# Kernel tuning notes

Hardware: AMD Instinct MI355X
Metric: run time of the kernel (lower is better)

Reference implementation:

```python
import jax, jax.numpy as jnp
import numpy as np

NEG_INF = -1e9  # stands in for the eye(W)*sys.maxsize self-mask on the row axis


def setup_inputs() -> dict:
    key = jax.random.key(0)
    ks = jax.random.split(key, 8)
    B, C, S = 8, 512, 128
    C8 = C // 8
    sc = 0.02
    x = jax.random.normal(ks[0], (B, C, S, S), dtype=jnp.float32)
    Wq = jax.random.normal(ks[1], (C8, C), dtype=jnp.float32) * sc
    bq = jnp.zeros((C8,), dtype=jnp.float32)
    Wk = jax.random.normal(ks[2], (C8, C), dtype=jnp.float32) * sc
    bk = jnp.zeros((C8,), dtype=jnp.float32)
    Wv = jax.random.normal(ks[3], (C, C), dtype=jnp.float32) * sc
    bv = jnp.zeros((C,), dtype=jnp.float32)
    gamma = jnp.ones((1,), dtype=jnp.float32) * 0.5  # source inits to 0; nonzero so path is exercised
    return {"x": x, "Wq": Wq, "bq": bq, "Wk": Wk, "bk": bk, "Wv": Wv, "bv": bv, "gamma": gamma}


def reference(x, Wq, bq, Wk, bk, Wv, bv, gamma):
    # x: (B, C, W, H) with W == H == S (required by the eye-mask view in the source)
    B, C, S, _ = x.shape
    # 1x1 convs = per-pixel linear projections
    q = jnp.einsum('oc,bcwh->bowh', Wq, x) + bq[None, :, None, None]  # (B,C8,S,S)
    k = jnp.einsum('oc,bcwh->bowh', Wk, x) + bk[None, :, None, None]
    v = jnp.einsum('oc,bcwh->bowh', Wv, x) + bv[None, :, None, None]  # (B,C,S,S)

    # column ('h'-fixed) attention along W, self position masked out
    e_col = jnp.einsum('bcwh,bcuh->bwhu', q, k)  # (B,W,H,W)
    self_mask = jnp.eye(S, dtype=bool)  # w == u
    e_col = jnp.where(self_mask[None, :, None, :], NEG_INF, e_col)
    # row ('w'-fixed) attention along H
    e_row = jnp.einsum('bcwh,bcwu->bwhu', q, k)  # (B,W,H,H)

    att = jax.nn.softmax(jnp.concatenate([e_col, e_row], axis=-1), axis=-1)  # (B,W,H,2S)
    a_col = att[..., :S]   # weights over w'
    a_row = att[..., S:]   # weights over h'

    out = (jnp.einsum('bwhu,bcuh->bcwh', a_col, v)
           + jnp.einsum('bwhu,bcwu->bcwh', a_row, v))  # (B,C,S,S)
    return gamma[0] * out + x
```

## Files before the change

kernel.cpp:

```cpp
#include <hip/hip_runtime.h>
#include <hip/hip_bf16.h>


#define S 128
#define SS 16384
#define C 512
#define C8 64
#define NEG_BIG -1000000000.0f

using short8 = __attribute__((ext_vector_type(8))) short;
using f32x4  = __attribute__((ext_vector_type(4))) float;

#define GPTR(p) ((const __attribute__((address_space(1))) void*)(p))
#define LPTR(p) ((__attribute__((address_space(3))) void*)(p))

__device__ __forceinline__ unsigned short f2b(float f){
  union { float f; unsigned u; } v; v.f = f;
  unsigned r = (v.u + 0x7fffu + ((v.u >> 16) & 1u)) >> 16;
  return (unsigned short)r;
}
__device__ __forceinline__ float b2f(unsigned short h){
  union { unsigned u; float f; } v; v.u = ((unsigned)h) << 16;
  return v.f;
}

__device__ __forceinline__ void stage_tile64(unsigned short* dst,
    const unsigned short* src, int tid){
  #pragma unroll
  for (int p = 0; p < 4; ++p){
    int gi = p * 256 + tid;
    int row = gi >> 3, cc = gi & 7;
    int kc = (cc ^ (row & 7)) * 8;
    __builtin_amdgcn_global_load_lds(GPTR(src + (size_t)row * C + kc),
                                     LPTR((char*)dst + gi * 16), 16, 0, 0);
  }
}

__global__ __launch_bounds__(256) void k_pack_w(
    const float* __restrict__ Wq, const float* __restrict__ Wk,
    const float* __restrict__ Wv, unsigned short* __restrict__ wall){
  int i = blockIdx.x * 256 + threadIdx.x;
  if (i >= 640 * C) return;
  int co = i >> 9, ci = i & (C - 1);
  float v;
  if (co < 64)        v = Wq[co * C + ci];
  else if (co < 128)  v = Wk[(co - 64) * C + ci];
  else                v = Wv[(co - 128) * C + ci];
  wall[i] = f2b(v);
}

__global__ __launch_bounds__(256) void k_xp(
    const float* __restrict__ x, unsigned short* __restrict__ xp){
  __shared__ unsigned short T[128 * 130] __attribute__((aligned(16)));
  int blk = blockIdx.x;
  int ct = blk & 3; int bw = blk >> 2;
  int w = bw & 127; int b = bw >> 7;
  int tid = threadIdx.x;
  int ci0 = ct * 128;
  const float* xb = x + ((size_t)(b * C + ci0) * S + w) * S;
  #pragma unroll
  for (int p = 0; p < 16; ++p){
    int idx = p * 256 + tid;
    int cc = idx >> 5;
    int h4 = (idx & 31) * 4;
    float4 v = *(const float4*)(xb + (size_t)cc * SS + h4);
    unsigned* d = (unsigned*)&T[cc * 130 + h4];
    d[0] = (unsigned)f2b(v.x) | ((unsigned)f2b(v.y) << 16);
    d[1] = (unsigned)f2b(v.z) | ((unsigned)f2b(v.w) << 16);
  }
  __syncthreads();
  unsigned short* xpb = xp + (size_t)(b * S + w) * S * C + ci0;
  #pragma unroll
  for (int p = 0; p < 8; ++p){
    int idx = p * 256 + tid;
    int h  = idx >> 4;
    int ch = (idx & 15) * 8;
    unsigned short tmp[8] __attribute__((aligned(16)));
    #pragma unroll
    for (int j = 0; j < 8; ++j) tmp[j] = T[(ch + j) * 130 + h];
    *(uint4*)(xpb + (size_t)h * C + ch) = *(uint4*)tmp;
  }
}

__global__ __launch_bounds__(256) void k_qkv(
    const unsigned short* __restrict__ xp, const unsigned short* __restrict__ wall,
    const float* __restrict__ bq, const float* __restrict__ bk,
    const float* __restrict__ bv,
    unsigned short* __restrict__ qp, unsigned short* __restrict__ kp,
    unsigned short* __restrict__ vb){
  __shared__ unsigned short sm[32768] __attribute__((aligned(16)));
  unsigned short* Dl = sm;
  int blk = blockIdx.x;
  int pxsub = blk & 7; int t = blk >> 3;
  int cot = t % 5; int pxg = t / 5;
  int pxt = pxg * 8 + pxsub;
  int w = pxt & 127, b = pxt >> 7;
  int tid = threadIdx.x, lane = tid & 63, wid = tid >> 6;
  int qd = lane >> 4, ln = lane & 15;
  const unsigned short* asrc0 = wall + (size_t)cot * 128 * C;
  const unsigned short* bsrc0 = xp + (size_t)pxt * 128 * C;
  f32x4 acc[4][4];
  #pragma unroll
  for (int i = 0; i < 4; ++i)
    #pragma unroll
    for (int j = 0; j < 4; ++j) acc[i][j] = (f32x4){0.f, 0.f, 0.f, 0.f};

  stage_tile64(sm,        asrc0, tid);
  stage_tile64(sm + 8192, bsrc0, tid);
  __syncthreads();

  for (int kw = 0; kw < 8; ++kw){
    unsigned short* Acur = sm + (kw & 1) * 16384;
    unsigned short* Bcur = Acur + 8192;
    if (kw < 7){
      unsigned short* Anxt = sm + ((kw + 1) & 1) * 16384;
      stage_tile64(Anxt,        asrc0 + (kw + 1) * 64, tid);
      stage_tile64(Anxt + 8192, bsrc0 + (kw + 1) * 64, tid);
    }
    __builtin_amdgcn_s_setprio(1);
    #pragma unroll
    for (int ks = 0; ks < 2; ++ks){
      int ch8 = (((ks * 4 + qd) ^ (ln & 7)) * 8);
      short8 af[4], bfr[4];
      #pragma unroll
      for (int i = 0; i < 4; ++i)
        af[i] = *(const short8*)&Acur[(((wid & 1) * 4 + i) * 16 + ln) * 64 + ch8];
      #pragma unroll
      for (int j = 0; j < 4; ++j)
        bfr[j] = *(const short8*)&Bcur[(((wid >> 1) * 4 + j) * 16 + ln) * 64 + ch8];
      #pragma unroll
      for (int i = 0; i < 4; ++i)
        #pragma unroll
        for (int j = 0; j < 4; ++j)
          acc[i][j] = __builtin_amdgcn_mfma_f32_16x16x32_bf16(af[i], bfr[j], acc[i][j], 0, 0, 0);
    }
    __builtin_amdgcn_s_setprio(0);
    __syncthreads();
  }
  float bias_[4][4];
  #pragma unroll
  for (int i = 0; i < 4; ++i){
    int co_l0 = ((wid & 1) * 4 + i) * 16 + qd * 4;
    #pragma unroll
    for (int r = 0; r < 4; ++r){
      int co_l = co_l0 + r;
      bias_[i][r] = (cot == 0) ? (co_l < 64 ? bq[co_l] : bk[co_l - 64])
                               : bv[(cot - 1) * 128 + co_l];
    }
  }
  #pragma unroll
  for (int i = 0; i < 4; ++i){
    int co_l0 = ((wid & 1) * 4 + i) * 16 + qd * 4;
    #pragma unroll
    for (int j = 0; j < 4; ++j){
      int pxl = ((wid >> 1) * 4 + j) * 16 + ln;
      #pragma unroll
      for (int r = 0; r < 4; ++r)
        Dl[(co_l0 + r) * 136 + pxl] = f2b(acc[i][j][r] + bias_[i][r]);
    }
  }
  __syncthreads();
  if (cot == 0){
    unsigned short* qb = qp + (size_t)(b * S + w) * S * C8;
    unsigned short* kb = kp + (size_t)(b * S + w) * S * C8;
    #pragma unroll
    for (int p = 0; p < 4; ++p){
      int idx = p * 256 + tid;
      int cch = idx & 7, hh = idx >> 3;
      unsigned short tq[8] __attribute__((aligned(16)));
      unsigned short tk[8] __attribute__((aligned(16)));
      #pragma unroll
      for (int jj = 0; jj < 8; ++jj){
        tq[jj] = Dl[(cch * 8 + jj) * 136 + hh];
        tk[jj] = Dl[(64 + cch * 8 + jj) * 136 + hh];
      }
      *(uint4*)(qb + (size_t)hh * C8 + cch * 8) = *(uint4*)tq;
      *(uint4*)(kb + (size_t)hh * C8 + cch * 8) = *(uint4*)tk;
    }
  } else {
    unsigned short* vbb = vb + ((size_t)(b * C + (cot - 1) * 128) * S + w) * S;
    #pragma unroll
    for (int p = 0; p < 8; ++p){
      int idx = p * 256 + tid;
      int c_l = idx >> 4, hc = (idx & 15) * 8;
      uint4 v = *(const uint4*)&Dl[c_l * 136 + hc];
      *(uint4*)(vbb + (size_t)c_l * SS + hc) = v;
    }
  }
}

__global__ __launch_bounds__(256) void k_tv(
    const unsigned short* __restrict__ vb, unsigned short* __restrict__ vt){
  __shared__ unsigned short T[128 * 130] __attribute__((aligned(16)));
  int bc = blockIdx.x;
  const unsigned short* src = vb + (size_t)bc * SS;
  unsigned short* dst = vt + (size_t)bc * SS;
  int tid = threadIdx.x;
  #pragma unroll
  for (int p = 0; p < 8; ++p){
    int idx = p * 256 + tid;
    int wv = idx >> 4, ch = (idx & 15) * 8;
    uint4 v = *(const uint4*)(src + wv * S + ch);
    unsigned* d = (unsigned*)&T[wv * 130 + ch];
    d[0] = v.x; d[1] = v.y; d[2] = v.z; d[3] = v.w;
  }
  __syncthreads();
  #pragma unroll
  for (int p = 0; p < 8; ++p){
    int idx = p * 256 + tid;
    int h = idx >> 4, ch = (idx & 15) * 8;
    unsigned short tmp[8] __attribute__((aligned(16)));
    #pragma unroll
    for (int j = 0; j < 8; ++j) tmp[j] = T[(ch + j) * 130 + h];
    *(uint4*)(dst + h * S + ch) = *(uint4*)tmp;
  }
}

__global__ __launch_bounds__(256) void k_ecol(
    const unsigned short* __restrict__ qp, const unsigned short* __restrict__ kp,
    unsigned short* __restrict__ eca){
  __shared__ unsigned short Aq[128 * 72] __attribute__((aligned(16)));
  __shared__ unsigned short Bk[128 * 72] __attribute__((aligned(16)));
  int blk = blockIdx.x; int h = blk & 127, b = blk >> 7;
  int tid = threadIdx.x, lane = tid & 63, wid = tid >> 6;
  int qd = lane >> 4, ln = lane & 15;
  #pragma unroll
  for (int p = 0; p < 4; ++p){
    int idx = p * 256 + tid;
    int row = idx >> 3, ch = (idx & 7) * 8;
    *(uint4*)&Aq[row * 72 + ch] = *(const uint4*)(qp + ((size_t)(b * S + row) * S + h) * C8 + ch);
    *(uint4*)&Bk[row * 72 + ch] = *(const uint4*)(kp + ((size_t)(b * S + row) * S + h) * C8 + ch);
  }
  __syncthreads();
  f32x4 acc[4][4];
  #pragma unroll
  for (int i = 0; i < 4; ++i)
    #pragma unroll
    for (int j = 0; j < 4; ++j) acc[i][j] = (f32x4){0.f, 0.f, 0.f, 0.f};
  #pragma unroll
  for (int ks = 0; ks < 2; ++ks){
    int ko = ks * 32 + qd * 8;
    short8 af[4], bfr[4];
    #pragma unroll
    for (int i = 0; i < 4; ++i)
      af[i] = *(const short8*)&Aq[(((wid & 1) * 4 + i) * 16 + ln) * 72 + ko];
    #pragma unroll
    for (int j = 0; j < 4; ++j)
      bfr[j] = *(const short8*)&Bk[(((wid >> 1) * 4 + j) * 16 + ln) * 72 + ko];
    #pragma unroll
    for (int i = 0; i < 4; ++i)
      #pragma unroll
      for (int j = 0; j < 4; ++j)
        acc[i][j] = __builtin_amdgcn_mfma_f32_16x16x32_bf16(af[i], bfr[j], acc[i][j], 0, 0, 0);
  }
  #pragma unroll
  for (int i = 0; i < 4; ++i){
    int w0 = ((wid & 1) * 4 + i) * 16 + qd * 4;
    #pragma unroll
    for (int j = 0; j < 4; ++j){
      int ug = ((wid >> 1) * 4 + j) * 16 + ln;
      #pragma unroll
      for (int r = 0; r < 4; ++r){
        int wg = w0 + r;
        float val = acc[i][j][r];
        if (wg == ug) val = NEG_BIG;
        eca[((size_t)(b * S + wg) * S + h) * S + ug] = f2b(val);
      }
    }
  }
}

__global__ __launch_bounds__(256) void k_erow_softmax(
    const unsigned short* __restrict__ qp, const unsigned short* __restrict__ kp,
    unsigned short* __restrict__ eca, unsigned short* __restrict__ ar){
  __shared__ char sm[36864] __attribute__((aligned(16)));
  unsigned short* Aq = (unsigned short*)sm;
  unsigned short* Bk = (unsigned short*)(sm + 18432);
  unsigned short* El = (unsigned short*)sm;
  float* redm = (float*)(sm + 34816);
  float* reds = (float*)(sm + 35840);
  int blk = blockIdx.x; int w = blk & 127, b = blk >> 7;
  int tid = threadIdx.x, lane = tid & 63, wid = tid >> 6;
  int qd = lane >> 4, ln = lane & 15;
  size_t tb = (size_t)(b * S + w) * SS;
  {
    const unsigned short* qsrc = qp + (size_t)(b * S + w) * S * C8;
    const unsigned short* ksrc = kp + (size_t)(b * S + w) * S * C8;
    #pragma unroll
    for (int p = 0; p < 4; ++p){
      int idx = p * 256 + tid;
      int row = idx >> 3, ch = (idx & 7) * 8;
      *(uint4*)&Aq[row * 72 + ch] = *(const uint4*)(qsrc + row * C8 + ch);
      *(uint4*)&Bk[row * 72 + ch] = *(const uint4*)(ksrc + row * C8 + ch);
    }
  }
  __syncthreads();
  f32x4 acc[4][4];
  #pragma unroll
  for (int i = 0; i < 4; ++i)
    #pragma unroll
    for (int j = 0; j < 4; ++j) acc[i][j] = (f32x4){0.f, 0.f, 0.f, 0.f};
  #pragma unroll
  for (int ks = 0; ks < 2; ++ks){
    int ko = ks * 32 + qd * 8;
    short8 af[4], bfr[4];
    #pragma unroll
    for (int i = 0; i < 4; ++i)
      af[i] = *(const short8*)&Aq[(((wid & 1) * 4 + i) * 16 + ln) * 72 + ko];
    #pragma unroll
    for (int j = 0; j < 4; ++j)
      bfr[j] = *(const short8*)&Bk[(((wid >> 1) * 4 + j) * 16 + ln) * 72 + ko];
    #pragma unroll
    for (int i = 0; i < 4; ++i)
      #pragma unroll
      for (int j = 0; j < 4; ++j)
        acc[i][j] = __builtin_amdgcn_mfma_f32_16x16x32_bf16(af[i], bfr[j], acc[i][j], 0, 0, 0);
  }
  __syncthreads();
  #pragma unroll
  for (int i = 0; i < 4; ++i){
    int h0 = ((wid & 1) * 4 + i) * 16 + qd * 4;
    #pragma unroll
    for (int j = 0; j < 4; ++j){
      int ul = ((wid >> 1) * 4 + j) * 16 + ln;
      #pragma unroll
      for (int r = 0; r < 4; ++r)
        El[(h0 + r) * 136 + ul] = f2b(acc[i][j][r]);
    }
  }
  __syncthreads();
  int h = tid >> 1, half = tid & 1;
  const uint4* src4 = (half == 0) ? (const uint4*)(eca + tb + (size_t)h * S)
                                  : (const uint4*)&El[h * 136];
  float mx = -3.0e38f;
  #pragma unroll 4
  for (int u = 0; u < 16; ++u){
    uint4 v = src4[u];
    const unsigned short* e = (const unsigned short*)&v;
    #pragma unroll
    for (int jj = 0; jj < 8; ++jj) mx = fmaxf(mx, b2f(e[jj]));
  }
  redm[tid] = mx;
  __syncthreads();
  float m = fmaxf(mx, redm[tid ^ 1]);
  float s = 0.f;
  #pragma unroll 4
  for (int u = 0; u < 16; ++u){
    uint4 v = src4[u];
    const unsigned short* e = (const unsigned short*)&v;
    #pragma unroll
    for (int jj = 0; jj < 8; ++jj) s += __expf(b2f(e[jj]) - m);
  }
  reds[tid] = s;
  __syncthreads();
  float inv = 1.0f / (s + reds[tid ^ 1]);
  uint4* dst4 = (half == 0) ? (uint4*)(eca + tb + (size_t)h * S)
                            : (uint4*)(ar + tb + (size_t)h * S);
  #pragma unroll 4
  for (int u = 0; u < 16; ++u){
    uint4 v = src4[u];
    const unsigned short* e = (const unsigned short*)&v;
    unsigned short o[8] __attribute__((aligned(16)));
    #pragma unroll
    for (int jj = 0; jj < 8; ++jj) o[jj] = f2b(__expf(b2f(e[jj]) - m) * inv);
    dst4[u] = *(uint4*)o;
  }
}

__global__ __launch_bounds__(256) void k_outrow(
    const unsigned short* __restrict__ vb, const unsigned short* __restrict__ ar,
    unsigned short* __restrict__ orw){
  __shared__ unsigned short Av[128 * 72] __attribute__((aligned(16)));
  __shared__ unsigned short Ba[128 * 72] __attribute__((aligned(16)));
  int blk = blockIdx.x;
  int ct = blk & 3; int bw = blk >> 2;
  int w = bw & 127, b = bw >> 7;
  int tid = threadIdx.x, lane = tid & 63, wid = tid >> 6;
  int qd = lane >> 4, ln = lane & 15;
  size_t tb = (size_t)(b * S + w) * SS;
  f32x4 acc[4][4];
  #pragma unroll
  for (int i = 0; i < 4; ++i)
    #pragma unroll
    for (int j = 0; j < 4; ++j) acc[i][j] = (f32x4){0.f, 0.f, 0.f, 0.f};
  for (int kw = 0; kw < 2; ++kw){
    __syncthreads();
    #pragma unroll
    for (int p = 0; p < 4; ++p){
      int idx = p * 256 + tid;
      int row = idx >> 3, ch = (idx & 7) * 8;
      *(uint4*)&Av[row * 72 + ch] =
        *(const uint4*)(vb + ((size_t)(b * C + ct * 128 + row) * S + w) * S + kw * 64 + ch);
      *(uint4*)&Ba[row * 72 + ch] =
        *(const uint4*)(ar + tb + (size_t)row * S + kw * 64 + ch);
    }
    __syncthreads();
    #pragma unroll
    for (int ks = 0; ks < 2; ++ks){
      int ko = ks * 32 + qd * 8;
      short8 af[4], bfr[4];
      #pragma unroll
      for (int i = 0; i < 4; ++i)
        af[i] = *(const short8*)&Av[(((wid & 1) * 4 + i) * 16 + ln) * 72 + ko];
      #pragma unroll
      for (int j = 0; j < 4; ++j)
        bfr[j] = *(const short8*)&Ba[(((wid >> 1) * 4 + j) * 16 + ln) * 72 + ko];
      #pragma unroll
      for (int i = 0; i < 4; ++i)
        #pragma unroll
        for (int j = 0; j < 4; ++j)
          acc[i][j] = __builtin_amdgcn_mfma_f32_16x16x32_bf16(af[i], bfr[j], acc[i][j], 0, 0, 0);
    }
  }
  #pragma unroll
  for (int i = 0; i < 4; ++i){
    int c0 = ((wid & 1) * 4 + i) * 16 + qd * 4;
    #pragma unroll
    for (int j = 0; j < 4; ++j){
      int hl = ((wid >> 1) * 4 + j) * 16 + ln;
      #pragma unroll
      for (int r = 0; r < 4; ++r){
        int cg = ct * 128 + c0 + r;
        orw[((size_t)(b * C + cg) * S + w) * S + hl] = f2b(acc[i][j][r]);
      }
    }
  }
}

__global__ __launch_bounds__(256) void k_outcol(
    const unsigned short* __restrict__ vt, const unsigned short* __restrict__ eca,
    unsigned short* __restrict__ oct){
  __shared__ unsigned short Av[128 * 72] __attribute__((aligned(16)));
  __shared__ unsigned short Ba[128 * 72] __attribute__((aligned(16)));
  int blk = blockIdx.x;
  int ct = blk & 3; int bh = blk >> 2;
  int h = bh & 127, b = bh >> 7;
  int tid = threadIdx.x, lane = tid & 63, wid = tid >> 6;
  int qd = lane >> 4, ln = lane & 15;
  f32x4 acc[4][4];
  #pragma unroll
  for (int i = 0; i < 4; ++i)
    #pragma unroll
    for (int j = 0; j < 4; ++j) acc[i][j] = (f32x4){0.f, 0.f, 0.f, 0.f};
  for (int kw = 0; kw < 2; ++kw){
    __syncthreads();
    #pragma unroll
    for (int p = 0; p < 4; ++p){
      int idx = p * 256 + tid;
      int row = idx >> 3, ch = (idx & 7) * 8;
      *(uint4*)&Av[row * 72 + ch] =
        *(const uint4*)(vt + ((size_t)(b * C + ct * 128 + row) * S + h) * S + kw * 64 + ch);
      *(uint4*)&Ba[row * 72 + ch] =
        *(const uint4*)(eca + ((size_t)(b * S + row) * S + h) * S + kw * 64 + ch);
    }
    __syncthreads();
    #pragma unroll
    for (int ks = 0; ks < 2; ++ks){
      int ko = ks * 32 + qd * 8;
      short8 af[4], bfr[4];
      #pragma unroll
      for (int i = 0; i < 4; ++i)
        af[i] = *(const short8*)&Av[(((wid & 1) * 4 + i) * 16 + ln) * 72 + ko];
      #pragma unroll
      for (int j = 0; j < 4; ++j)
        bfr[j] = *(const short8*)&Ba[(((wid >> 1) * 4 + j) * 16 + ln) * 72 + ko];
      #pragma unroll
      for (int i = 0; i < 4; ++i)
        #pragma unroll
        for (int j = 0; j < 4; ++j)
          acc[i][j] = __builtin_amdgcn_mfma_f32_16x16x32_bf16(af[i], bfr[j], acc[i][j], 0, 0, 0);
    }
  }
  #pragma unroll
  for (int i = 0; i < 4; ++i){
    int c0 = ((wid & 1) * 4 + i) * 16 + qd * 4;
    #pragma unroll
    for (int j = 0; j < 4; ++j){
      int wl = ((wid >> 1) * 4 + j) * 16 + ln;
      #pragma unroll
      for (int r = 0; r < 4; ++r){
        int cg = ct * 128 + c0 + r;
        oct[((size_t)(b * S + h) * C + cg) * S + wl] = f2b(acc[i][j][r]);
      }
    }
  }
}

__global__ __launch_bounds__(256) void k_final(
    const unsigned short* __restrict__ oct, const unsigned short* __restrict__ orw,
    const float* __restrict__ x, const float* __restrict__ gamma,
    float* __restrict__ out){
  __shared__ unsigned short T[128 * 130] __attribute__((aligned(16)));
  int blk = blockIdx.x;
  int c = blk & 511, b = blk >> 9;
  int tid = threadIdx.x;
  float g = gamma[0];
  #pragma unroll
  for (int p = 0; p < 8; ++p){
    int idx = p * 256 + tid;
    int hh = idx >> 4, ch = (idx & 15) * 8;
    uint4 v = *(const uint4*)(oct + ((size_t)(b * S + hh) * C + c) * S + ch);
    unsigned* d = (unsigned*)&T[hh * 130 + ch];
    d[0] = v.x; d[1] = v.y; d[2] = v.z; d[3] = v.w;
  }
  __syncthreads();
  #pragma unroll
  for (int p = 0; p < 8; ++p){
    int idx = p * 256 + tid;
    int wv = idx >> 4, hch = (idx & 15) * 8;
    size_t o = ((size_t)(b * C + c) * S + wv) * S + hch;
    uint4 rv = *(const uint4*)(orw + o);
    const unsigned short* rr = (const unsigned short*)&rv;
    float4 x0 = *(const float4*)(x + o);
    float4 x1 = *(const float4*)(x + o + 4);
    float4 o0, o1;
    o0.x = g * (b2f(rr[0]) + b2f(T[(hch + 0) * 130 + wv])) + x0.x;
    o0.y = g * (b2f(rr[1]) + b2f(T[(hch + 1) * 130 + wv])) + x0.y;
    o0.z = g * (b2f(rr[2]) + b2f(T[(hch + 2) * 130 + wv])) + x0.z;
    o0.w = g * (b2f(rr[3]) + b2f(T[(hch + 3) * 130 + wv])) + x0.w;
    o1.x = g * (b2f(rr[4]) + b2f(T[(hch + 4) * 130 + wv])) + x1.x;
    o1.y = g * (b2f(rr[5]) + b2f(T[(hch + 5) * 130 + wv])) + x1.y;
    o1.z = g * (b2f(rr[6]) + b2f(T[(hch + 6) * 130 + wv])) + x1.z;
    o1.w = g * (b2f(rr[7]) + b2f(T[(hch + 7) * 130 + wv])) + x1.w;
    *(float4*)(out + o) = o0;
    *(float4*)(out + o + 4) = o1;
  }
}

extern "C" void kernel_launch(void* const* d_in, const int* in_sizes, int n_in,
                              void* d_out, int out_size, void* d_ws, size_t ws_size,
                              hipStream_t stream){
  const float* x     = (const float*)d_in[0];
  const float* Wq    = (const float*)d_in[1];
  const float* bq    = (const float*)d_in[2];
  const float* Wk    = (const float*)d_in[3];
  const float* bk    = (const float*)d_in[4];
  const float* Wv    = (const float*)d_in[5];
  const float* bv    = (const float*)d_in[6];
  const float* gamma = (const float*)d_in[7];
  float* out = (float*)d_out;
  char* ws = (char*)d_ws;

  const size_t OFF_WALL = 0;
  const size_t OFF_XP   = 1ull << 20;
  const size_t OFF_QP   = OFF_XP  + 134217728ull;
  const size_t OFF_KP   = OFF_QP  + 16777216ull;
  const size_t OFF_VB   = OFF_KP  + 16777216ull;
  const size_t OFF_VT   = OFF_VB  + 134217728ull;
  const size_t OFF_ECA  = OFF_VT  + 134217728ull;
  const size_t OFF_AR   = OFF_ECA + 33554432ull;
  const size_t OFF_OCT  = OFF_XP;
  const size_t OFF_ORW  = OFF_VT;
  const size_t NEED     = OFF_AR + 33554432ull;
  if (ws_size < NEED) return;

  unsigned short* wall = (unsigned short*)(ws + OFF_WALL);
  unsigned short* xp   = (unsigned short*)(ws + OFF_XP);
  unsigned short* qp   = (unsigned short*)(ws + OFF_QP);
  unsigned short* kp   = (unsigned short*)(ws + OFF_KP);
  unsigned short* vb   = (unsigned short*)(ws + OFF_VB);
  unsigned short* vt   = (unsigned short*)(ws + OFF_VT);
  unsigned short* eca  = (unsigned short*)(ws + OFF_ECA);
  unsigned short* ar   = (unsigned short*)(ws + OFF_AR);
  unsigned short* oct  = (unsigned short*)(ws + OFF_OCT);
  unsigned short* orw  = (unsigned short*)(ws + OFF_ORW);

  k_pack_w      <<<1280, 256, 0, stream>>>(Wq, Wk, Wv, wall);
  k_xp          <<<4096, 256, 0, stream>>>(x, xp);
  k_qkv         <<<5120, 256, 0, stream>>>(xp, wall, bq, bk, bv, qp, kp, vb);
  k_tv          <<<4096, 256, 0, stream>>>(vb, vt);
  k_ecol        <<<1024, 256, 0, stream>>>(qp, kp, eca);
  k_erow_softmax<<<1024, 256, 0, stream>>>(qp, kp, eca, ar);
  k_outcol      <<<4096, 256, 0, stream>>>(vt, eca, oct);
  k_outrow      <<<4096, 256, 0, stream>>>(vb, ar, orw);
  k_final       <<<4096, 256, 0, stream>>>(oct, orw, x, gamma, out);
}
```

Baseline: 987.6 us.

## Fuse row softmax with row-attention output GEMM and permute transpose rows

The row-energy softmax kernel now keeps the normalized row attention weights in shared memory and immediately runs the V·A_row GEMM across all channel tiles. V tiles are double-buffered via global_load_lds, and the result is written in place over vb. This removes the separate k_outrow launch, the round trip of the `ar` buffer through global memory, and the repeated reloads of attention weights. Separately, the LDS transpose buffers use a row permutation (PR) to reduce bank conflicts. The costs are roughly 70KB of LDS per block, which lowers occupancy, and in-place overwriting of vb that depends on each block reading only its own w-slice.

```diff
diff --git a/kernel.cpp b/kernel.cpp
--- a/kernel.cpp
+++ b/kernel.cpp
@@ -14,6 +14,8 @@
 #define GPTR(p) ((const __attribute__((address_space(1))) void*)(p))
 #define LPTR(p) ((__attribute__((address_space(3))) void*)(p))
 
+#define PR(r) ((((r) & 7) << 4) | ((r) >> 3))
+
 __device__ __forceinline__ unsigned short f2b(float f){
   union { float f; unsigned u; } v; v.f = f;
   unsigned r = (v.u + 0x7fffu + ((v.u >> 16) & 1u)) >> 16;
@@ -25,13 +27,13 @@
 }
 
 __device__ __forceinline__ void stage_tile64(unsigned short* dst,
-    const unsigned short* src, int tid){
+    const unsigned short* src, size_t rstride, int tid){
   #pragma unroll
   for (int p = 0; p < 4; ++p){
     int gi = p * 256 + tid;
     int row = gi >> 3, cc = gi & 7;
     int kc = (cc ^ (row & 7)) * 8;
-    __builtin_amdgcn_global_load_lds(GPTR(src + (size_t)row * C + kc),
+    __builtin_amdgcn_global_load_lds(GPTR(src + (size_t)row * rstride + kc),
                                      LPTR((char*)dst + gi * 16), 16, 0, 0);
   }
 }
@@ -64,7 +66,7 @@
     int cc = idx >> 5;
     int h4 = (idx & 31) * 4;
     float4 v = *(const float4*)(xb + (size_t)cc * SS + h4);
-    unsigned* d = (unsigned*)&T[cc * 130 + h4];
+    unsigned* d = (unsigned*)&T[PR(cc) * 130 + h4];
     d[0] = (unsigned)f2b(v.x) | ((unsigned)f2b(v.y) << 16);
     d[1] = (unsigned)f2b(v.z) | ((unsigned)f2b(v.w) << 16);
   }
@@ -77,7 +79,7 @@
     int ch = (idx & 15) * 8;
     unsigned short tmp[8] __attribute__((aligned(16)));
     #pragma unroll
-    for (int j = 0; j < 8; ++j) tmp[j] = T[(ch + j) * 130 + h];
+    for (int j = 0; j < 8; ++j) tmp[j] = T[PR(ch + j) * 130 + h];
     *(uint4*)(xpb + (size_t)h * C + ch) = *(uint4*)tmp;
   }
 }
@@ -105,8 +107,8 @@
     #pragma unroll
     for (int j = 0; j < 4; ++j) acc[i][j] = (f32x4){0.f, 0.f, 0.f, 0.f};
 
-  stage_tile64(sm,        asrc0, tid);
-  stage_tile64(sm + 8192, bsrc0, tid);
+  stage_tile64(sm,        asrc0, C, tid);
+  stage_tile64(sm + 8192, bsrc0, C, tid);
   __syncthreads();
 
   for (int kw = 0; kw < 8; ++kw){
@@ -114,8 +116,8 @@
     unsigned short* Bcur = Acur + 8192;
     if (kw < 7){
       unsigned short* Anxt = sm + ((kw + 1) & 1) * 16384;
-      stage_tile64(Anxt,        asrc0 + (kw + 1) * 64, tid);
-      stage_tile64(Anxt + 8192, bsrc0 + (kw + 1) * 64, tid);
+      stage_tile64(Anxt,        asrc0 + (kw + 1) * 64, C, tid);
+      stage_tile64(Anxt + 8192, bsrc0 + (kw + 1) * 64, C, tid);
     }
     __builtin_amdgcn_s_setprio(1);
     #pragma unroll
@@ -201,7 +203,7 @@
     int idx = p * 256 + tid;
     int wv = idx >> 4, ch = (idx & 15) * 8;
     uint4 v = *(const uint4*)(src + wv * S + ch);
-    unsigned* d = (unsigned*)&T[wv * 130 + ch];
+    unsigned* d = (unsigned*)&T[PR(wv) * 130 + ch];
     d[0] = v.x; d[1] = v.y; d[2] = v.z; d[3] = v.w;
   }
   __syncthreads();
@@ -211,7 +213,7 @@
     int h = idx >> 4, ch = (idx & 15) * 8;
     unsigned short tmp[8] __attribute__((aligned(16)));
     #pragma unroll
-    for (int j = 0; j < 8; ++j) tmp[j] = T[(ch + j) * 130 + h];
+    for (int j = 0; j < 8; ++j) tmp[j] = T[PR(ch + j) * 130 + h];
     *(uint4*)(dst + h * S + ch) = *(uint4*)tmp;
   }
 }
@@ -270,19 +272,23 @@
   }
 }
 
-__global__ __launch_bounds__(256) void k_erow_softmax(
+__global__ __launch_bounds__(256) void k_erow_sm_outrow(
     const unsigned short* __restrict__ qp, const unsigned short* __restrict__ kp,
-    unsigned short* __restrict__ eca, unsigned short* __restrict__ ar){
-  __shared__ char sm[36864] __attribute__((aligned(16)));
-  unsigned short* Aq = (unsigned short*)sm;
-  unsigned short* Bk = (unsigned short*)(sm + 18432);
-  unsigned short* El = (unsigned short*)sm;
-  float* redm = (float*)(sm + 34816);
-  float* reds = (float*)(sm + 35840);
+    unsigned short* __restrict__ eca, unsigned short* vb){
+  __shared__ char sm[71680] __attribute__((aligned(16)));
+  unsigned short* Aq  = (unsigned short*)sm;
+  unsigned short* Bk  = (unsigned short*)(sm + 18432);
+  unsigned short* El  = (unsigned short*)sm;
+  unsigned short* Av0 = (unsigned short*)(sm + 36864);
+  unsigned short* Av1 = (unsigned short*)(sm + 53248);
+  float* redm = (float*)(sm + 69632);
+  float* reds = (float*)(sm + 70656);
   int blk = blockIdx.x; int w = blk & 127, b = blk >> 7;
   int tid = threadIdx.x, lane = tid & 63, wid = tid >> 6;
   int qd = lane >> 4, ln = lane & 15;
   size_t tb = (size_t)(b * S + w) * SS;
+  const unsigned short* vsrc0 = vb + (size_t)(b * C) * SS + (size_t)w * S;
+
   {
     const unsigned short* qsrc = qp + (size_t)(b * S + w) * S * C8;
     const unsigned short* ksrc = kp + (size_t)(b * S + w) * S * C8;
@@ -294,6 +300,7 @@
       *(uint4*)&Bk[row * 72 + ch] = *(const uint4*)(ksrc + row * C8 + ch);
     }
   }
+  stage_tile64(Av0, vsrc0, SS, tid);
   __syncthreads();
   f32x4 acc[4][4];
   #pragma unroll
@@ -329,101 +336,95 @@
     }
   }
   __syncthreads();
-  int h = tid >> 1, half = tid & 1;
-  const uint4* src4 = (half == 0) ? (const uint4*)(eca + tb + (size_t)h * S)
-                                  : (const uint4*)&El[h * 136];
-  float mx = -3.0e38f;
-  #pragma unroll 4
-  for (int u = 0; u < 16; ++u){
-    uint4 v = src4[u];
-    const unsigned short* e = (const unsigned short*)&v;
-    #pragma unroll
-    for (int jj = 0; jj < 8; ++jj) mx = fmaxf(mx, b2f(e[jj]));
-  }
-  redm[tid] = mx;
-  __syncthreads();
-  float m = fmaxf(mx, redm[tid ^ 1]);
-  float s = 0.f;
-  #pragma unroll 4
-  for (int u = 0; u < 16; ++u){
-    uint4 v = src4[u];
-    const unsigned short* e = (const unsigned short*)&v;
-    #pragma unroll
-    for (int jj = 0; jj < 8; ++jj) s += __expf(b2f(e[jj]) - m);
-  }
-  reds[tid] = s;
-  __syncthreads();
-  float inv = 1.0f / (s + reds[tid ^ 1]);
-  uint4* dst4 = (half == 0) ? (uint4*)(eca + tb + (size_t)h * S)
-                            : (uint4*)(ar + tb + (size_t)h * S);
-  #pragma unroll 4
-  for (int u = 0; u < 16; ++u){
-    uint4 v = src4[u];
-    const unsigned short* e = (const unsigned short*)&v;
-    unsigned short o[8] __attribute__((aligned(16)));
-    #pragma unroll
-    for (int jj = 0; jj < 8; ++jj) o[jj] = f2b(__expf(b2f(e[jj]) - m) * inv);
-    dst4[u] = *(uint4*)o;
-  }
-}
-
-__global__ __launch_bounds__(256) void k_outrow(
-    const unsigned short* __restrict__ vb, const unsigned short* __restrict__ ar,
-    unsigned short* __restrict__ orw){
-  __shared__ unsigned short Av[128 * 72] __attribute__((aligned(16)));
-  __shared__ unsigned short Ba[128 * 72] __attribute__((aligned(16)));
-  int blk = blockIdx.x;
-  int ct = blk & 3; int bw = blk >> 2;
-  int w = bw & 127, b = bw >> 7;
-  int tid = threadIdx.x, lane = tid & 63, wid = tid >> 6;
-  int qd = lane >> 4, ln = lane & 15;
-  size_t tb = (size_t)(b * S + w) * SS;
-  f32x4 acc[4][4];
-  #pragma unroll
-  for (int i = 0; i < 4; ++i)
-    #pragma unroll
-    for (int j = 0; j < 4; ++j) acc[i][j] = (f32x4){0.f, 0.f, 0.f, 0.f};
-  for (int kw = 0; kw < 2; ++kw){
+  {
+    int h = tid >> 1, half = tid & 1;
+    const uint4* src4 = (half == 0) ? (const uint4*)(eca + tb + (size_t)h * S)
+                                    : (const uint4*)&El[h * 136];
+    float mx = -3.0e38f;
+    #pragma unroll 4
+    for (int u = 0; u < 16; ++u){
+      uint4 v = src4[u];
+      const unsigned short* e = (const unsigned short*)&v;
+      #pragma unroll
+      for (int jj = 0; jj < 8; ++jj) mx = fmaxf(mx, b2f(e[jj]));
+    }
+    redm[tid] = mx;
     __syncthreads();
-    #pragma unroll
-    for (int p = 0; p < 4; ++p){
-      int idx = p * 256 + tid;
-      int row = idx >> 3, ch = (idx & 7) * 8;
-      *(uint4*)&Av[row * 72 + ch] =
-        *(const uint4*)(vb + ((size_t)(b * C + ct * 128 + row) * S + w) * S + kw * 64 + ch);
-      *(uint4*)&Ba[row * 72 + ch] =
-        *(const uint4*)(ar + tb + (size_t)row * S + kw * 64 + ch);
-    }
+    float m = fmaxf(mx, redm[tid ^ 1]);
+    float s = 0.f;
+    #pragma unroll 4
+    for (int u = 0; u < 16; ++u){
+      uint4 v = src4[u];
+      const unsigned short* e = (const unsigned short*)&v;
+      #pragma unroll
+      for (int jj = 0; jj < 8; ++jj) s += __expf(b2f(e[jj]) - m);
+    }
+    reds[tid] = s;
     __syncthreads();
+    float inv = 1.0f / (s + reds[tid ^ 1]);
+    uint4* dst4 = (half == 0) ? (uint4*)(eca + tb + (size_t)h * S)
+                              : (uint4*)&El[h * 136];
+    #pragma unroll 4
+    for (int u = 0; u < 16; ++u){
+      uint4 v = src4[u];
+      const unsigned short* e = (const unsigned short*)&v;
+      unsigned short o[8] __attribute__((aligned(16)));
+      #pragma unroll
+      for (int jj = 0; jj < 8; ++jj) o[jj] = f2b(__expf(b2f(e[jj]) - m) * inv);
+      dst4[u] = *(uint4*)o;
+    }
+  }
+  __syncthreads();
+
+  for (int s = 0; s < 8; ++s){
+    int ct = s >> 1, kw = s & 1;
+    unsigned short* Acur = (s & 1) ? Av1 : Av0;
+    if (s < 7){
+      int ct1 = (s + 1) >> 1, kw1 = (s + 1) & 1;
+      stage_tile64((s & 1) ? Av0 : Av1,
+                   vsrc0 + (size_t)(ct1 * 128) * SS + kw1 * 64, SS, tid);
+    }
+    if (kw == 0){
+      #pragma unroll
+      for (int i = 0; i < 4; ++i)
+        #pragma unroll
+        for (int j = 0; j < 4; ++j) acc[i][j] = (f32x4){0.f, 0.f, 0.f, 0.f};
+    }
+    __builtin_amdgcn_s_setprio(1);
     #pragma unroll
     for (int ks = 0; ks < 2; ++ks){
-      int ko = ks * 32 + qd * 8;
+      int ch8 = (((ks * 4 + qd) ^ (ln & 7)) * 8);
+      int ko = kw * 64 + ks * 32 + qd * 8;
       short8 af[4], bfr[4];
       #pragma unroll
       for (int i = 0; i < 4; ++i)
-        af[i] = *(const short8*)&Av[(((wid & 1) * 4 + i) * 16 + ln) * 72 + ko];
+        af[i] = *(const short8*)&Acur[(((wid & 1) * 4 + i) * 16 + ln) * 64 + ch8];
       #pragma unroll
       for (int j = 0; j < 4; ++j)
-        bfr[j] = *(const short8*)&Ba[(((wid >> 1) * 4 + j) * 16 + ln) * 72 + ko];
+        bfr[j] = *(const short8*)&El[(((wid >> 1) * 4 + j) * 16 + ln) * 136 + ko];
       #pragma unroll
       for (int i = 0; i < 4; ++i)
         #pragma unroll
         for (int j = 0; j < 4; ++j)
           acc[i][j] = __builtin_amdgcn_mfma_f32_16x16x32_bf16(af[i], bfr[j], acc[i][j], 0, 0, 0);
     }
-  }
-  #pragma unroll
-  for (int i = 0; i < 4; ++i){
-    int c0 = ((wid & 1) * 4 + i) * 16 + qd * 4;
-    #pragma unroll
-    for (int j = 0; j < 4; ++j){
-      int hl = ((wid >> 1) * 4 + j) * 16 + ln;
-      #pragma unroll
-      for (int r = 0; r < 4; ++r){
-        int cg = ct * 128 + c0 + r;
-        orw[((size_t)(b * C + cg) * S + w) * S + hl] = f2b(acc[i][j][r]);
+    __builtin_amdgcn_s_setprio(0);
+    if (kw == 1){
+      #pragma unroll
+      for (int i = 0; i < 4; ++i){
+        int c0 = ((wid & 1) * 4 + i) * 16 + qd * 4;
+        #pragma unroll
+        for (int j = 0; j < 4; ++j){
+          int hl = ((wid >> 1) * 4 + j) * 16 + ln;
+          #pragma unroll
+          for (int r = 0; r < 4; ++r){
+            int cg = ct * 128 + c0 + r;
+            vb[((size_t)(b * C + cg) * S + w) * S + hl] = f2b(acc[i][j][r]);
+          }
+        }
       }
     }
+    __syncthreads();
   }
 }
 
@@ -500,7 +501,7 @@
     int idx = p * 256 + tid;
     int hh = idx >> 4, ch = (idx & 15) * 8;
     uint4 v = *(const uint4*)(oct + ((size_t)(b * S + hh) * C + c) * S + ch);
-    unsigned* d = (unsigned*)&T[hh * 130 + ch];
+    unsigned* d = (unsigned*)&T[PR(hh) * 130 + ch];
     d[0] = v.x; d[1] = v.y; d[2] = v.z; d[3] = v.w;
   }
   __syncthreads();
@@ -514,14 +515,14 @@
     float4 x0 = *(const float4*)(x + o);
     float4 x1 = *(const float4*)(x + o + 4);
     float4 o0, o1;
-    o0.x = g * (b2f(rr[0]) + b2f(T[(hch + 0) * 130 + wv])) + x0.x;
-    o0.y = g * (b2f(rr[1]) + b2f(T[(hch + 1) * 130 + wv])) + x0.y;
-    o0.z = g * (b2f(rr[2]) + b2f(T[(hch + 2) * 130 + wv])) + x0.z;
-    o0.w = g * (b2f(rr[3]) + b2f(T[(hch + 3) * 130 + wv])) + x0.w;
-    o1.x = g * (b2f(rr[4]) + b2f(T[(hch + 4) * 130 + wv])) + x1.x;
-    o1.y = g * (b2f(rr[5]) + b2f(T[(hch + 5) * 130 + wv])) + x1.y;
-    o1.z = g * (b2f(rr[6]) + b2f(T[(hch + 6) * 130 + wv])) + x1.z;
-    o1.w = g * (b2f(rr[7]) + b2f(T[(hch + 7) * 130 + wv])) + x1.w;
+    o0.x = g * (b2f(rr[0]) + b2f(T[PR(hch + 0) * 130 + wv])) + x0.x;
+    o0.y = g * (b2f(rr[1]) + b2f(T[PR(hch + 1) * 130 + wv])) + x0.y;
+    o0.z = g * (b2f(rr[2]) + b2f(T[PR(hch + 2) * 130 + wv])) + x0.z;
+    o0.w = g * (b2f(rr[3]) + b2f(T[PR(hch + 3) * 130 + wv])) + x0.w;
+    o1.x = g * (b2f(rr[4]) + b2f(T[PR(hch + 4) * 130 + wv])) + x1.x;
+    o1.y = g * (b2f(rr[5]) + b2f(T[PR(hch + 5) * 130 + wv])) + x1.y;
+    o1.z = g * (b2f(rr[6]) + b2f(T[PR(hch + 6) * 130 + wv])) + x1.z;
+    o1.w = g * (b2f(rr[7]) + b2f(T[PR(hch + 7) * 130 + wv])) + x1.w;
     *(float4*)(out + o) = o0;
     *(float4*)(out + o + 4) = o1;
   }
@@ -548,10 +549,8 @@
   const size_t OFF_VB   = OFF_KP  + 16777216ull;
   const size_t OFF_VT   = OFF_VB  + 134217728ull;
   const size_t OFF_ECA  = OFF_VT  + 134217728ull;
-  const size_t OFF_AR   = OFF_ECA + 33554432ull;
   const size_t OFF_OCT  = OFF_XP;
-  const size_t OFF_ORW  = OFF_VT;
-  const size_t NEED     = OFF_AR + 33554432ull;
+  const size_t NEED     = OFF_ECA + 33554432ull;
   if (ws_size < NEED) return;
 
   unsigned short* wall = (unsigned short*)(ws + OFF_WALL);
@@ -561,17 +560,14 @@
   unsigned short* vb   = (unsigned short*)(ws + OFF_VB);
   unsigned short* vt   = (unsigned short*)(ws + OFF_VT);
   unsigned short* eca  = (unsigned short*)(ws + OFF_ECA);
-  unsigned short* ar   = (unsigned short*)(ws + OFF_AR);
   unsigned short* oct  = (unsigned short*)(ws + OFF_OCT);
-  unsigned short* orw  = (unsigned short*)(ws + OFF_ORW);
-
-  k_pack_w      <<<1280, 256, 0, stream>>>(Wq, Wk, Wv, wall);
-  k_xp          <<<4096, 256, 0, stream>>>(x, xp);
-  k_qkv         <<<5120, 256, 0, stream>>>(xp, wall, bq, bk, bv, qp, kp, vb);
-  k_tv          <<<4096, 256, 0, stream>>>(vb, vt);
-  k_ecol        <<<1024, 256, 0, stream>>>(qp, kp, eca);
-  k_erow_softmax<<<1024, 256, 0, stream>>>(qp, kp, eca, ar);
-  k_outcol      <<<4096, 256, 0, stream>>>(vt, eca, oct);
-  k_outrow      <<<4096, 256, 0, stream>>>(vb, ar, orw);
-  k_final       <<<4096, 256, 0, stream>>>(oct, orw, x, gamma, out);
-}
+
+  k_pack_w        <<<1280, 256, 0, stream>>>(Wq, Wk, Wv, wall);
+  k_xp            <<<4096, 256, 0, stream>>>(x, xp);
+  k_qkv           <<<5120, 256, 0, stream>>>(xp, wall, bq, bk, bv, qp, kp, vb);
+  k_tv            <<<4096, 256, 0, stream>>>(vb, vt);
+  k_ecol          <<<1024, 256, 0, stream>>>(qp, kp, eca);
+  k_erow_sm_outrow<<<1024, 256, 0, stream>>>(qp, kp, eca, vb);
+  k_outcol        <<<4096, 256, 0, stream>>>(vt, eca, oct);
+  k_final         <<<4096, 256, 0, stream>>>(oct, vb, x, gamma, out);
+}
```

Measured after the change: 921.2 us. 1.07x faster.
